# Performance work log

Hardware: AMD Instinct MI355X
Metric: run time of the kernel (lower is better)

The kernel has to match this reference:

```python
import jax, jax.numpy as jnp
import numpy as np

COND_SIZE = 512
LR_SCALE = 1.0 / np.sqrt(COND_SIZE)  # equalized-lr scale for the style linear
EPS = 1e-8


def _style(condition, w):
    # lr_equal(nn.Linear(cond_size, in_size, bias=False)): runtime weight scale 1/sqrt(fan_in)
    return (condition @ w.T) * LR_SCALE  # [B, Cin]


def _mod_demod_conv(x, w, b, style):
    # x [B,Cin,H,W], w [Cout,Cin,3,3], style [B,Cin]
    wmod = w[None] * style[:, None, :, None, None]               # [B,Cout,Cin,3,3]
    demod = jax.lax.rsqrt(jnp.sum(wmod * wmod, axis=(2, 3, 4)) + EPS)  # [B,Cout]
    wmod = wmod * demod[:, :, None, None, None]
    conv1 = lambda xi, wi: jax.lax.conv_general_dilated(
        xi[None], wi, window_strides=(1, 1), padding='SAME')[0]
    out = jax.vmap(conv1)(x, wmod)                                # per-sample weights
    return out + b[None, :, None, None]


def setup_inputs() -> dict:
    key = jax.random.key(0)
    ks = jax.random.split(key, 12)
    B, Cin, Cout, H, W = 8, 128, 64, 256, 256
    return {
        'inputs': jax.random.normal(ks[0], (B, Cin, H, W), jnp.float32),
        'condition': jax.random.normal(ks[1], (B, COND_SIZE), jnp.float32),
        'cond_w0': jax.random.normal(ks[2], (Cin, COND_SIZE), jnp.float32),
        'cond_w1': jax.random.normal(ks[3], (Cin, COND_SIZE), jnp.float32),
        'conv_w0': jax.random.normal(ks[4], (Cin, Cin, 3, 3), jnp.float32) * 0.05,
        'conv_b0': jnp.zeros((Cin,), jnp.float32),
        'conv_w1': jax.random.normal(ks[5], (Cout, Cin, 3, 3), jnp.float32) * 0.05,
        'conv_b1': jnp.zeros((Cout,), jnp.float32),
        'noise_scale0': jax.random.normal(ks[6], (Cin,), jnp.float32),
        'noise_scale1': jax.random.normal(ks[7], (Cout,), jnp.float32),
        'noise0': jax.random.normal(ks[8], (B, Cin, H, W), jnp.float32),
        'noise1': jax.random.normal(ks[9], (B, Cout, H, W), jnp.float32),
        'rgb_w': jax.random.normal(ks[10], (3, Cout), jnp.float32) * 0.05,
        'rgb_b': jnp.zeros((3,), jnp.float32),
    }


def reference(inputs, condition, cond_w0, cond_w1, conv_w0, conv_b0,
              conv_w1, conv_b1, noise_scale0, noise_scale1,
              noise0, noise1, rgb_w, rgb_b):
    # block 0: modulated/demodulated 3x3 conv + channel-scaled noise injection
    out = _mod_demod_conv(inputs, conv_w0, conv_b0, _style(condition, cond_w0))
    out = out + noise0 * noise_scale0[None, :, None, None]
    # block 1
    out = _mod_demod_conv(out, conv_w1, conv_b1, _style(condition, cond_w1))
    out = out + noise1 * noise_scale1[None, :, None, None]
    # 1x1 to-RGB conv
    rgb = jnp.einsum('bchw,oc->bohw', out, rgb_w) + rgb_b[None, :, None, None]
    return (out, rgb)
```

## Files before the change

kernel.cpp:

```cpp
#include <hip/hip_runtime.h>
#include <stdint.h>
#include <stddef.h>


typedef __bf16 bf16;
typedef __bf16 bf16x8 __attribute__((ext_vector_type(8)));
typedef float  f32x4  __attribute__((ext_vector_type(4)));

#define AS1 __attribute__((address_space(1)))
#define AS3 __attribute__((address_space(3)))

#define OFF_A1    0ull
#define OFF_WT0   134217728ull
#define OFF_WT1   134512640ull
#define OFF_S0    134660096ull
#define OFF_S1    134664192ull
#define OFF_DM0   134668288ull
#define OFF_DM1   134672384ull
#define OFF_WSQ0  134674432ull
#define OFF_WSQ1  134739968ull
#define OFF_ZP    134772736ull

static __device__ __forceinline__ void gload_lds16(const void* src, void* ldsdst) {
  __builtin_amdgcn_global_load_lds((const AS1 void*)src, (AS3 void*)ldsdst, 16, 0, 0);
}

__global__ __launch_bounds__(256) void k_prep1(
    const float* __restrict__ cond, const float* __restrict__ cw0,
    const float* __restrict__ cw1, const float* __restrict__ w0,
    const float* __restrict__ w1, float* __restrict__ s0, float* __restrict__ s1,
    bf16* __restrict__ wt0, bf16* __restrict__ wt1,
    float* __restrict__ wsq0, float* __restrict__ wsq1, float* __restrict__ zp)
{
  int idx = blockIdx.x * 256 + threadIdx.x;
  if (idx < 2048) {
    int which = idx >> 10; int b = (idx >> 7) & 7; int c = idx & 127;
    const float* cw = which ? cw1 : cw0;
    const float* cp = cond + b * 512;
    const float* wp = cw + c * 512;
    float acc = 0.f;
    for (int j = 0; j < 512; ++j) acc += cp[j] * wp[j];
    (which ? s1 : s0)[b * 128 + c] = acc * 0.044194173824159216f;
    return;
  }
  idx -= 2048;
  if (idx < 147456) {
    int t = idx >> 14;
    wt0[idx] = (bf16)w0[(idx & 16383) * 9 + t];
    return;
  }
  idx -= 147456;
  if (idx < 73728) {
    int t = idx >> 13;
    wt1[idx] = (bf16)w1[(idx & 8191) * 9 + t];
    return;
  }
  idx -= 73728;
  if (idx < 16384) {
    const float* p = w0 + idx * 9; float a = 0.f;
    #pragma unroll
    for (int t = 0; t < 9; ++t) a += p[t] * p[t];
    wsq0[idx] = a; return;
  }
  idx -= 16384;
  if (idx < 8192) {
    const float* p = w1 + idx * 9; float a = 0.f;
    #pragma unroll
    for (int t = 0; t < 9; ++t) a += p[t] * p[t];
    wsq1[idx] = a; return;
  }
  idx -= 8192;
  if (idx < 64) zp[idx] = 0.f;
}

__global__ __launch_bounds__(256) void k_prep2(
    const float* __restrict__ s0, const float* __restrict__ s1,
    const float* __restrict__ wsq0, const float* __restrict__ wsq1,
    float* __restrict__ dm0, float* __restrict__ dm1)
{
  int idx = blockIdx.x * 256 + threadIdx.x;
  if (idx < 1024) {
    int b = idx >> 7, co = idx & 127;
    const float* sp = s0 + b * 128; const float* wp = wsq0 + co * 128;
    float a = 0.f;
    for (int ci = 0; ci < 128; ++ci) { float s = sp[ci]; a += s * s * wp[ci]; }
    dm0[idx] = rsqrtf(a + 1e-8f);
  } else if (idx < 1536) {
    int j = idx - 1024; int b = j >> 6, co = j & 63;
    const float* sp = s1 + b * 128; const float* wp = wsq1 + co * 128;
    float a = 0.f;
    for (int ci = 0; ci < 128; ++ci) { float s = sp[ci]; a += s * s * wp[ci]; }
    dm1[j] = rsqrtf(a + 1e-8f);
  }
}

__global__ __launch_bounds__(256) void k_mod(
    const float* __restrict__ x, const float* __restrict__ s0, bf16* __restrict__ A0)
{
  __shared__ alignas(16) char lds[8192];
  int bid = blockIdx.x;
  int b = bid >> 11; int rem = bid & 2047; int h = rem >> 3; int wp0 = (rem & 7) << 5;
  int t = threadIdx.x;
  #pragma unroll
  for (int iter = 0; iter < 2; ++iter) {
    int idx = iter * 256 + t; int w = idx & 31; int chunk = idx >> 5;
    const float* xp = x + (((size_t)(b * 128 + chunk * 8)) << 16) + (h << 8) + wp0 + w;
    const float* sp = s0 + b * 128 + chunk * 8;
    bf16x8 v;
    #pragma unroll
    for (int i = 0; i < 8; ++i) v[i] = (bf16)(xp[(size_t)i << 16] * sp[i]);
    *(bf16x8*)(lds + w * 256 + ((chunk ^ (w & 7)) << 4)) = v;
  }
  __syncthreads();
  #pragma unroll
  for (int iter = 0; iter < 2; ++iter) {
    int idx = iter * 256 + t; int w = idx >> 4; int c = idx & 15;
    bf16x8 v = *(const bf16x8*)(lds + w * 256 + ((c ^ (w & 7)) << 4));
    *(bf16x8*)(A0 + ((((size_t)(b << 16)) + (h << 8) + wp0 + w) << 7) + (c << 3)) = v;
  }
}

constexpr int cDY[9] = {0,0,0,1,1,1,2,2,2};
constexpr int cDX[9] = {0,1,2,0,1,2,0,1,2};

static __device__ __forceinline__ void stage_tileA(
    const bf16* __restrict__ src, const bf16* __restrict__ zp, char* Abase,
    int b, int h0, int w0p, int wave, int lane)
{
  #pragma unroll
  for (int i = 0; i < 12; ++i) {
    int g = wave + (i << 2);
    if (g < 45) {
      int pin = (g << 2) + (lane >> 4); int j = lane & 15;
      int r = pin / 18; int c = pin - r * 18;
      int gh = h0 - 1 + r, gw = w0p - 1 + c;
      const bf16* s;
      if (((unsigned)gh < 256u) & ((unsigned)gw < 256u))
        s = src + ((((size_t)(b << 16)) + (gh << 8) + gw) << 7) + ((j ^ (pin & 7)) << 3);
      else
        s = zp;
      gload_lds16(s, Abase + (size_t)g * 1024);
    }
  }
}

__global__ __launch_bounds__(256, 2) void k_conv0(
    const bf16* __restrict__ A0, const bf16* __restrict__ wt,
    const float* __restrict__ dm, const float* __restrict__ bias,
    const float* __restrict__ noise, const float* __restrict__ nsc,
    const float* __restrict__ s1, const bf16* __restrict__ zp,
    bf16* __restrict__ A1)
{
  extern __shared__ __align__(16) char lds[];
  char* Abase = lds;
  char* Bp[4] = { lds + 46080, lds + 54272, lds + 62464, lds + 70656 };

  int bid = blockIdx.x;
  int wg = (bid & 7) * 512 + (bid >> 3);
  int b = wg >> 9; int rem = wg & 511;
  int h0 = (rem >> 4) << 3; int w0p = (rem & 15) << 4;
  int tid = threadIdx.x; int wave = tid >> 6; int lane = tid & 63;

  auto stageB = [&](int s, char* dst) {
    const int t = s >> 2, ci = (s & 3) << 5;
    #pragma unroll
    for (int i = 0; i < 2; ++i) {
      int co_base = (wave << 4) + (i << 6);
      int co = co_base + (lane >> 2);
      int kgs = (lane & 3) ^ ((co >> 1) & 3);
      gload_lds16(wt + ((size_t)t << 14) + co * 128 + ci + (kgs << 3),
                  dst + co_base * 64);
    }
  };

  stage_tileA(A0, zp, Abase, b, h0, w0p, wave, lane);
  stageB(0, Bp[0]);
  stageB(1, Bp[1]);
  asm volatile("s_waitcnt vmcnt(0)" ::: "memory");
  __builtin_amdgcn_s_barrier();

  int m16 = lane & 15, kg = lane >> 4;
  int pb = (wave >> 1) << 6, cb = (wave & 1) << 6;
  int basePin[4];
  #pragma unroll
  for (int mr = 0; mr < 4; ++mr)
    basePin[mr] = ((pb >> 4) + mr) * 18 + m16;

  f32x4 acc[4][4] = {};
  #pragma unroll
  for (int p = 0; p < 18; ++p) {
    if (p + 1 < 18) {
      stageB(2 * (p + 1),     Bp[((p + 1) & 1) * 2]);
      stageB(2 * (p + 1) + 1, Bp[((p + 1) & 1) * 2 + 1]);
    }
    #pragma unroll
    for (int sub = 0; sub < 2; ++sub) {
      const int s = 2 * p + sub;
      char* Bcur = Bp[(p & 1) * 2 + sub];
      const int t = s >> 2, c4 = s & 3;
      const int dy = cDY[t], dx = cDX[t];
      bf16x8 a[4], bwv[4];
      #pragma unroll
      for (int nr = 0; nr < 4; ++nr) {
        int co = cb + nr * 16 + m16;
        int slot = kg ^ ((co >> 1) & 3);
        bwv[nr] = *(const bf16x8*)(Bcur + co * 64 + (slot << 4));
      }
      #pragma unroll
      for (int mr = 0; mr < 4; ++mr) {
        int pin = basePin[mr] + dy * 18 + dx;
        int cc = (c4 << 2) + kg;
        a[mr] = *(const bf16x8*)(Abase + pin * 256 + ((cc ^ (pin & 7)) << 4));
      }
      __builtin_amdgcn_s_setprio(1);
      #pragma unroll
      for (int mr = 0; mr < 4; ++mr)
        #pragma unroll
        for (int nr = 0; nr < 4; ++nr)
          acc[mr][nr] = __builtin_amdgcn_mfma_f32_16x16x32_bf16(
              a[mr], bwv[nr], acc[mr][nr], 0, 0, 0);
      __builtin_amdgcn_s_setprio(0);
    }
    if (p < 17) {
      asm volatile("s_waitcnt vmcnt(0)" ::: "memory");
      __builtin_amdgcn_s_barrier();
    }
  }
  __syncthreads();

  float* zl = (float*)lds;
  #pragma unroll
  for (int half = 0; half < 2; ++half) {
    if ((wave >> 1) == half) {
      #pragma unroll
      for (int nr = 0; nr < 4; ++nr) {
        int co = cb + nr * 16 + m16;
        float d = dm[(b << 7) + co], bb = bias[co];
        #pragma unroll
        for (int mr = 0; mr < 4; ++mr) {
          int p0 = mr * 16 + (kg << 2);
          #pragma unroll
          for (int r = 0; r < 4; ++r)
            zl[(p0 + r) * 129 + co] = acc[mr][nr][r] * d + bb;
        }
      }
    }
    __syncthreads();
    #pragma unroll 4
    for (int it = 0; it < 32; ++it) {
      int idx = it * 256 + tid; int co = idx >> 6; int p6 = idx & 63;
      int gh = h0 + (half << 2) + (p6 >> 4), gw = w0p + (p6 & 15);
      float n = noise[(((size_t)((b << 7) + co)) << 16) + (gh << 8) + gw];
      float y = zl[p6 * 129 + co] + n * nsc[co];
      zl[p6 * 129 + co] = y * s1[(b << 7) + co];
    }
    __syncthreads();
    #pragma unroll
    for (int it = 0; it < 4; ++it) {
      int idx = it * 256 + tid; int p6 = idx >> 4; int ch = idx & 15;
      int gh = h0 + (half << 2) + (p6 >> 4), gw = w0p + (p6 & 15);
      const float* zpt = zl + p6 * 129 + (ch << 3);
      bf16x8 v;
      #pragma unroll
      for (int i = 0; i < 8; ++i) v[i] = (bf16)zpt[i];
      *(bf16x8*)(A1 + ((((size_t)(b << 16)) + (gh << 8) + gw) << 7) + (ch << 3)) = v;
    }
    __syncthreads();
  }
}

__global__ __launch_bounds__(256, 2) void k_conv1(
    const bf16* __restrict__ A1, const bf16* __restrict__ wt,
    const float* __restrict__ dm, const float* __restrict__ bias,
    const float* __restrict__ noise, const float* __restrict__ nsc,
    const float* __restrict__ rgbw, const float* __restrict__ rgbb,
    const bf16* __restrict__ zp, float* __restrict__ out, float* __restrict__ rgb)
{
  __shared__ alignas(16) char lds[62464];
  char* Abase = lds;
  char* Bp[4] = { lds + 46080, lds + 50176, lds + 54272, lds + 58368 };

  int bid = blockIdx.x;
  int wg = (bid & 7) * 512 + (bid >> 3);
  int b = wg >> 9; int rem = wg & 511;
  int h0 = (rem >> 4) << 3; int w0p = (rem & 15) << 4;
  int tid = threadIdx.x; int wave = tid >> 6; int lane = tid & 63;

  auto stageB = [&](int s, char* dst) {
    const int t = s >> 2, ci = (s & 3) << 5;
    int co_base = wave << 4;
    int co = co_base + (lane >> 2);
    int kgs = (lane & 3) ^ ((co >> 1) & 3);
    gload_lds16(wt + ((size_t)t << 13) + co * 128 + ci + (kgs << 3),
                dst + co_base * 64);
  };

  stage_tileA(A1, zp, Abase, b, h0, w0p, wave, lane);
  stageB(0, Bp[0]);
  stageB(1, Bp[1]);
  asm volatile("s_waitcnt vmcnt(0)" ::: "memory");
  __builtin_amdgcn_s_barrier();

  int m16 = lane & 15, kg = lane >> 4;
  int pb = (wave >> 1) << 6, cb = (wave & 1) << 5;
  int basePin[4];
  #pragma unroll
  for (int mr = 0; mr < 4; ++mr)
    basePin[mr] = ((pb >> 4) + mr) * 18 + m16;

  f32x4 acc[4][2] = {};
  #pragma unroll
  for (int p = 0; p < 18; ++p) {
    if (p + 1 < 18) {
      stageB(2 * (p + 1),     Bp[((p + 1) & 1) * 2]);
      stageB(2 * (p + 1) + 1, Bp[((p + 1) & 1) * 2 + 1]);
    }
    #pragma unroll
    for (int sub = 0; sub < 2; ++sub) {
      const int s = 2 * p + sub;
      char* Bcur = Bp[(p & 1) * 2 + sub];
      const int t = s >> 2, c4 = s & 3;
      const int dy = cDY[t], dx = cDX[t];
      bf16x8 a[4], bwv[2];
      #pragma unroll
      for (int nr = 0; nr < 2; ++nr) {
        int co = cb + nr * 16 + m16;
        int slot = kg ^ ((co >> 1) & 3);
        bwv[nr] = *(const bf16x8*)(Bcur + co * 64 + (slot << 4));
      }
      #pragma unroll
      for (int mr = 0; mr < 4; ++mr) {
        int pin = basePin[mr] + dy * 18 + dx;
        int cc = (c4 << 2) + kg;
        a[mr] = *(const bf16x8*)(Abase + pin * 256 + ((cc ^ (pin & 7)) << 4));
      }
      __builtin_amdgcn_s_setprio(1);
      #pragma unroll
      for (int mr = 0; mr < 4; ++mr)
        #pragma unroll
        for (int nr = 0; nr < 2; ++nr)
          acc[mr][nr] = __builtin_amdgcn_mfma_f32_16x16x32_bf16(
              a[mr], bwv[nr], acc[mr][nr], 0, 0, 0);
      __builtin_amdgcn_s_setprio(0);
    }
    if (p < 17) {
      asm volatile("s_waitcnt vmcnt(0)" ::: "memory");
      __builtin_amdgcn_s_barrier();
    }
  }
  __syncthreads();

  float nz[32];
  #pragma unroll
  for (int it = 0; it < 32; ++it) {
    int idx = it * 256 + tid; int co = idx >> 7; int px = idx & 127;
    int gh = h0 + (px >> 4), gw = w0p + (px & 15);
    nz[it] = noise[(((size_t)((b << 6) + co)) << 16) + (gh << 8) + gw];
  }
  float* zl = (float*)lds;
  #pragma unroll
  for (int nr = 0; nr < 2; ++nr) {
    int co = cb + nr * 16 + m16;
    float d = dm[(b << 6) + co], bb = bias[co];
    #pragma unroll
    for (int mr = 0; mr < 4; ++mr) {
      int p0 = pb + mr * 16 + (kg << 2);
      #pragma unroll
      for (int r = 0; r < 4; ++r)
        zl[(p0 + r) * 65 + co] = acc[mr][nr][r] * d + bb;
    }
  }
  __syncthreads();
  #pragma unroll
  for (int it = 0; it < 32; ++it) {
    int idx = it * 256 + tid; int co = idx >> 7; int px = idx & 127;
    int gh = h0 + (px >> 4), gw = w0p + (px & 15);
    size_t go = (((size_t)((b << 6) + co)) << 16) + (gh << 8) + gw;
    float y = zl[px * 65 + co] + nz[it] * nsc[co];
    zl[px * 65 + co] = y;
    out[go] = y;
  }
  __syncthreads();
  if (tid < 128) {
    int px = tid; int gh = h0 + (px >> 4), gw = w0p + (px & 15);
    float r0 = rgbb[0], r1 = rgbb[1], r2 = rgbb[2];
    for (int co = 0; co < 64; ++co) {
      float v = zl[px * 65 + co];
      r0 += v * rgbw[co]; r1 += v * rgbw[64 + co]; r2 += v * rgbw[128 + co];
    }
    size_t base = (((size_t)(b * 3)) << 16) + (gh << 8) + gw;
    rgb[base] = r0; rgb[base + (1 << 16)] = r1; rgb[base + (2 << 16)] = r2;
  }
}

extern "C" void kernel_launch(void* const* d_in, const int* in_sizes, int n_in,
                              void* d_out, int out_size, void* d_ws, size_t ws_size,
                              hipStream_t stream)
{
  const float* x      = (const float*)d_in[0];
  const float* cond   = (const float*)d_in[1];
  const float* cw0    = (const float*)d_in[2];
  const float* cw1    = (const float*)d_in[3];
  const float* w0     = (const float*)d_in[4];
  const float* b0     = (const float*)d_in[5];
  const float* w1     = (const float*)d_in[6];
  const float* b1     = (const float*)d_in[7];
  const float* ns0    = (const float*)d_in[8];
  const float* ns1    = (const float*)d_in[9];
  const float* noise0 = (const float*)d_in[10];
  const float* noise1 = (const float*)d_in[11];
  const float* rgbw   = (const float*)d_in[12];
  const float* rgbb   = (const float*)d_in[13];

  char* ws = (char*)d_ws;
  bf16*  A1   = (bf16*)(ws + OFF_A1);
  bf16*  WT0  = (bf16*)(ws + OFF_WT0);
  bf16*  WT1  = (bf16*)(ws + OFF_WT1);
  float* S0   = (float*)(ws + OFF_S0);
  float* S1   = (float*)(ws + OFF_S1);
  float* DM0  = (float*)(ws + OFF_DM0);
  float* DM1  = (float*)(ws + OFF_DM1);
  float* WSQ0 = (float*)(ws + OFF_WSQ0);
  float* WSQ1 = (float*)(ws + OFF_WSQ1);
  float* ZP   = (float*)(ws + OFF_ZP);

  float* out = (float*)d_out;
  float* rgb = out + 33554432;

  bf16* A0 = (bf16*)d_out;

  hipFuncSetAttribute((const void*)k_conv0,
                      hipFuncAttributeMaxDynamicSharedMemorySize, 78848);

  k_prep1<<<dim3(969), dim3(256), 0, stream>>>(cond, cw0, cw1, w0, w1,
                                               S0, S1, WT0, WT1, WSQ0, WSQ1, ZP);
  k_prep2<<<dim3(6), dim3(256), 0, stream>>>(S0, S1, WSQ0, WSQ1, DM0, DM1);
  k_mod<<<dim3(16384), dim3(256), 0, stream>>>(x, S0, A0);
  k_conv0<<<dim3(4096), dim3(256), 78848, stream>>>(A0, WT0, DM0, b0, noise0, ns0,
                                                    S1, (const bf16*)ZP, A1);
  k_conv1<<<dim3(4096), dim3(256), 0, stream>>>(A1, WT1, DM1, b1, noise1, ns1,
                                                rgbw, rgbb, (const bf16*)ZP, out, rgb);
}
```

Measured before the change: 465.3 us.

## Fuse input modulation and bf16 NHWC repack into conv0 halo staging

Removes the separate k_mod kernel, which scaled the fp32 NCHW input by the style and wrote a bf16 channels-last copy. conv0 now reads the fp32 input directly for its 10x18 halo tile, multiplies by the style, converts to bf16 and writes the swizzled LDS tile itself. This saves the intermediate write and re-read of the bf16 activation tensor and one launch. In exchange, halo pixels are re-read from fp32 across neighbouring tiles, the loads are strided per channel and synchronous instead of async global-to-LDS, and there is no overlap with the weight prefetch beyond the two initial B stages.

```diff
diff --git a/kernel.cpp b/kernel.cpp
--- a/kernel.cpp
+++ b/kernel.cpp
@@ -94,32 +94,6 @@
   }
 }
 
-__global__ __launch_bounds__(256) void k_mod(
-    const float* __restrict__ x, const float* __restrict__ s0, bf16* __restrict__ A0)
-{
-  __shared__ alignas(16) char lds[8192];
-  int bid = blockIdx.x;
-  int b = bid >> 11; int rem = bid & 2047; int h = rem >> 3; int wp0 = (rem & 7) << 5;
-  int t = threadIdx.x;
-  #pragma unroll
-  for (int iter = 0; iter < 2; ++iter) {
-    int idx = iter * 256 + t; int w = idx & 31; int chunk = idx >> 5;
-    const float* xp = x + (((size_t)(b * 128 + chunk * 8)) << 16) + (h << 8) + wp0 + w;
-    const float* sp = s0 + b * 128 + chunk * 8;
-    bf16x8 v;
-    #pragma unroll
-    for (int i = 0; i < 8; ++i) v[i] = (bf16)(xp[(size_t)i << 16] * sp[i]);
-    *(bf16x8*)(lds + w * 256 + ((chunk ^ (w & 7)) << 4)) = v;
-  }
-  __syncthreads();
-  #pragma unroll
-  for (int iter = 0; iter < 2; ++iter) {
-    int idx = iter * 256 + t; int w = idx >> 4; int c = idx & 15;
-    bf16x8 v = *(const bf16x8*)(lds + w * 256 + ((c ^ (w & 7)) << 4));
-    *(bf16x8*)(A0 + ((((size_t)(b << 16)) + (h << 8) + wp0 + w) << 7) + (c << 3)) = v;
-  }
-}
-
 constexpr int cDY[9] = {0,0,0,1,1,1,2,2,2};
 constexpr int cDX[9] = {0,1,2,0,1,2,0,1,2};
 
@@ -145,10 +119,10 @@
 }
 
 __global__ __launch_bounds__(256, 2) void k_conv0(
-    const bf16* __restrict__ A0, const bf16* __restrict__ wt,
-    const float* __restrict__ dm, const float* __restrict__ bias,
-    const float* __restrict__ noise, const float* __restrict__ nsc,
-    const float* __restrict__ s1, const bf16* __restrict__ zp,
+    const float* __restrict__ x, const bf16* __restrict__ wt,
+    const float* __restrict__ s0, const float* __restrict__ dm,
+    const float* __restrict__ bias, const float* __restrict__ noise,
+    const float* __restrict__ nsc, const float* __restrict__ s1,
     bf16* __restrict__ A1)
 {
   extern __shared__ __align__(16) char lds[];
@@ -173,11 +147,29 @@
     }
   };
 
-  stage_tileA(A0, zp, Abase, b, h0, w0p, wave, lane);
   stageB(0, Bp[0]);
   stageB(1, Bp[1]);
-  asm volatile("s_waitcnt vmcnt(0)" ::: "memory");
-  __builtin_amdgcn_s_barrier();
+
+  {
+    const float* sb = s0 + (b << 7);
+    for (int task = tid; task < 2880; task += 256) {
+      int j = task / 180; int pin = task - j * 180;
+      int r = pin / 18;  int c = pin - r * 18;
+      int gh = h0 - 1 + r, gw = w0p - 1 + c;
+      bf16x8 v;
+      if (((unsigned)gh < 256u) & ((unsigned)gw < 256u)) {
+        const float* xp = x + (((size_t)((b << 7) + (j << 3))) << 16) + (gh << 8) + gw;
+        #pragma unroll
+        for (int i = 0; i < 8; ++i)
+          v[i] = (bf16)(xp[(size_t)i << 16] * sb[(j << 3) + i]);
+      } else {
+        #pragma unroll
+        for (int i = 0; i < 8; ++i) v[i] = (bf16)0.f;
+      }
+      *(bf16x8*)(Abase + pin * 256 + ((j ^ (pin & 7)) << 4)) = v;
+    }
+  }
+  __syncthreads();
 
   int m16 = lane & 15, kg = lane >> 4;
   int pb = (wave >> 1) << 6, cb = (wave & 1) << 6;
@@ -427,17 +419,14 @@
   float* out = (float*)d_out;
   float* rgb = out + 33554432;
 
-  bf16* A0 = (bf16*)d_out;
-
   hipFuncSetAttribute((const void*)k_conv0,
                       hipFuncAttributeMaxDynamicSharedMemorySize, 78848);
 
   k_prep1<<<dim3(969), dim3(256), 0, stream>>>(cond, cw0, cw1, w0, w1,
                                                S0, S1, WT0, WT1, WSQ0, WSQ1, ZP);
   k_prep2<<<dim3(6), dim3(256), 0, stream>>>(S0, S1, WSQ0, WSQ1, DM0, DM1);
-  k_mod<<<dim3(16384), dim3(256), 0, stream>>>(x, S0, A0);
-  k_conv0<<<dim3(4096), dim3(256), 78848, stream>>>(A0, WT0, DM0, b0, noise0, ns0,
-                                                    S1, (const bf16*)ZP, A1);
+  k_conv0<<<dim3(4096), dim3(256), 78848, stream>>>(x, WT0, S0, DM0, b0, noise0,
+                                                    ns0, S1, A1);
   k_conv1<<<dim3(4096), dim3(256), 0, stream>>>(A1, WT1, DM1, b1, noise1, ns1,
                                                 rgbw, rgbb, (const bf16*)ZP, out, rgb);
 }
```

Measured after the change: 455.7 us (median of 2 runs). 1.02x faster.
